# Kernel tuning notes

Measured on AMD Instinct MI355X. Metric: run time of the kernel, lower is better.

## Reference

```python
import jax, jax.numpy as jnp
import numpy as np

N_NODES, N_EDGES, F_IN = 8192, 32768, 16
N_SUB, N_GRAPH = 512, 32
EDGE_DIM, HID = 5, 128
DIMS = [(16, 32), (32, 64), (64, 64)]  # (M_in, M_out) per NNConv layer


def _segment_mean(x, seg, n):
    s = jax.ops.segment_sum(x, seg, num_segments=n)
    c = jax.ops.segment_sum(jnp.ones((x.shape[0], 1), x.dtype), seg, num_segments=n)
    return s / jnp.maximum(c, 1.0)


def _nnconv(x, src, dst, eattr, W1, b1, W2, b2, root, bias):
    # edge MLP -> per-edge weight matrix theta: [E, M_in, M_out]
    h = jax.nn.relu(eattr @ W1 + b1)
    theta = (h @ W2 + b2).reshape(-1, x.shape[1], root.shape[1])
    msg = jnp.einsum('ei,eio->eo', x[src], theta)          # gather + per-edge matvec
    agg = jax.ops.segment_sum(msg, dst, num_segments=x.shape[0])  # scatter-add (aggr='add')
    return agg + x @ root + bias


def setup_inputs() -> dict:
    key = jax.random.key(0)
    ks = jax.random.split(key, 32)
    inp = {}
    inp['x'] = jax.random.normal(ks[0], (N_NODES, F_IN), jnp.float32)
    inp['edge_index'] = jax.random.randint(ks[1], (2, N_EDGES), 0, N_NODES)
    inp['edge_attr'] = jax.random.uniform(ks[2], (N_EDGES, EDGE_DIM), jnp.float32)
    inp['node_to_subgraph'] = jnp.sort(jax.random.randint(ks[3], (N_NODES,), 0, N_SUB))
    inp['subgraph_to_graph'] = jnp.sort(jax.random.randint(ks[4], (N_SUB,), 0, N_GRAPH))
    i = 5
    for l, (ci, co) in enumerate(DIMS):
        inp[f'W1_{l}'] = jax.random.normal(ks[i], (EDGE_DIM, HID), jnp.float32) * 0.1
        inp[f'b1_{l}'] = jnp.zeros((HID,), jnp.float32)
        inp[f'W2_{l}'] = jax.random.normal(ks[i + 1], (HID, ci * co), jnp.float32) * 0.05
        inp[f'b2_{l}'] = jnp.zeros((ci * co,), jnp.float32)
        inp[f'root_{l}'] = jax.random.normal(ks[i + 2], (ci, co), jnp.float32) * 0.1
        inp[f'bias_{l}'] = jnp.zeros((co,), jnp.float32)
        i += 3
    inp['fc1_w'] = jax.random.normal(ks[i], (64, 32), jnp.float32) * 0.1
    inp['fc1_b'] = jnp.zeros((32,), jnp.float32)
    inp['fc2_w'] = jax.random.normal(ks[i + 1], (32, 16), jnp.float32) * 0.1
    inp['fc2_b'] = jnp.zeros((16,), jnp.float32)
    inp['fc3_w'] = jax.random.normal(ks[i + 2], (16, 1), jnp.float32) * 0.1
    inp['fc3_b'] = jnp.zeros((1,), jnp.float32)
    return inp


def reference(x, edge_index, edge_attr, node_to_subgraph, subgraph_to_graph,
              W1_0, b1_0, W2_0, b2_0, root_0, bias_0,
              W1_1, b1_1, W2_1, b2_1, root_1, bias_1,
              W1_2, b1_2, W2_2, b2_2, root_2, bias_2,
              fc1_w, fc1_b, fc2_w, fc2_b, fc3_w, fc3_b):
    src, dst = edge_index[0], edge_index[1]
    layers = [(W1_0, b1_0, W2_0, b2_0, root_0, bias_0),
              (W1_1, b1_1, W2_1, b2_1, root_1, bias_1),
              (W1_2, b1_2, W2_2, b2_2, root_2, bias_2)]
    h = x
    for (W1, b1, W2, b2, root, bias) in layers:
        h = jax.nn.elu(_nnconv(h, src, dst, edge_attr, W1, b1, W2, b2, root, bias))
    h = _segment_mean(h, node_to_subgraph, N_SUB)      # global_mean_pool over subgraphs
    h = _segment_mean(h, subgraph_to_graph, N_GRAPH)   # global_mean_pool over graphs
    h = jax.nn.elu(h @ fc1_w + fc1_b)
    h = jax.nn.elu(h @ fc2_w + fc2_b)
    return (h @ fc3_w + fc3_b).reshape(-1)
```

## Files before the change

kernel.cpp:

```cpp
#include <hip/hip_runtime.h>

#define E_EDGES 32768
#define NN 8192
#define HID 128

typedef _Float16 half8 __attribute__((ext_vector_type(8)));
typedef _Float16 half4 __attribute__((ext_vector_type(4)));
typedef float f32x4 __attribute__((ext_vector_type(4)));

__device__ __forceinline__ void prep_one(int idx, int l2ci, int l2co,
                                         const float* __restrict__ W2,
                                         const float* __restrict__ b2,
                                         _Float16* __restrict__ out) {
  int CI = 1 << l2ci, CO = 1 << l2co;
  int Kmain = CI << 7;
  int j = idx & 7;
  int n = (idx >> 3) & (CO - 1);
  int kg = idx >> (3 + l2co);
  int k = kg * 8 + j;
  float v = 0.f;
  if (k < Kmain) {
    int hh = k >> l2ci, i = k & (CI - 1);
    v = W2[((hh << l2ci) + i) * CO + n];
  } else if (k < Kmain + CI) {
    v = b2[(k - Kmain) * CO + n];
  }
  out[idx] = (_Float16)v;
}

#define ZTOT (8192 * 32 + 8192 * 64 + 8192 * 64 + 512 * 64)
#define PREP0 (2176 * 32)
#define PREP1 (4224 * 64)
#define PREP2 (8320 * 64)

__global__ void prep_k(float* __restrict__ zr,
                       const float* __restrict__ W2a, const float* __restrict__ b2a, _Float16* __restrict__ oa,
                       const float* __restrict__ W2b, const float* __restrict__ b2b, _Float16* __restrict__ ob,
                       const float* __restrict__ W2c, const float* __restrict__ b2c, _Float16* __restrict__ oc) {
  int idx = blockIdx.x * 256 + threadIdx.x;
  if (idx < ZTOT) { zr[idx] = 0.f; return; }
  idx -= ZTOT;
  if (idx < PREP0) prep_one(idx, 4, 5, W2a, b2a, oa);
  else if (idx < PREP0 + PREP1) prep_one(idx - PREP0, 5, 6, W2b, b2b, ob);
  else if (idx < PREP0 + PREP1 + PREP2) prep_one(idx - PREP0 - PREP1, 6, 6, W2c, b2c, oc);
}

template <int CI, int CO>
__launch_bounds__(256, 2)
__global__ void msg_mfma_k(const float* __restrict__ xcur, const int* __restrict__ src,
                           const int* __restrict__ dst, const float* __restrict__ eattr,
                           const float* __restrict__ W1, const float* __restrict__ b1,
                           const _Float16* __restrict__ Bsw, float* __restrict__ agg) {
  constexpr int ME = 256;
  constexpr int L2CI = (CI == 64) ? 6 : ((CI == 32) ? 5 : 4);
  constexpr int Kmain = 128 * CI;
  constexpr int SPLITK = 32 * CI;
  constexpr int TAILK = ((SPLITK + CI + 127) / 128) * 128;
  constexpr int XSTR = CI + 8;
  constexpr int FC = CO / 16;
  constexpr int C4 = CI / 4;
  constexpr int L2C4 = L2CI - 2;
  constexpr int NV = (CI == 64) ? 2 : 1;

  __shared__ _Float16 he_s[32 * ME];
  __shared__ _Float16 xs_s[ME * XSTR];
  __shared__ float ea_s[ME * 5];
  __shared__ float W1s[5 * 32];
  __shared__ float b1s[32];
  __shared__ int src_s[ME];
  __shared__ int dst_s[ME];

  int t = threadIdx.x;
  int e0 = blockIdx.x * ME;
  int y = blockIdx.y;
  int hbeg = y * 32;

  for (int j = t; j < ME * 5; j += 256) ea_s[j] = eattr[e0 * 5 + j];
  if (t < 5 * 32) W1s[t] = W1[(t >> 5) * HID + hbeg + (t & 31)];
  if (t < 32) b1s[t] = b1[hbeg + t];
  src_s[t] = src[e0 + t];
  dst_s[t] = dst[e0 + t];
  __syncthreads();

  for (int j = t; j < 32 * ME; j += 256) {
    int hl = j >> 8, e = j & (ME - 1);
    float v = b1s[hl];
#pragma unroll
    for (int d = 0; d < 5; ++d) v += ea_s[e * 5 + d] * W1s[d * 32 + hl];
    he_s[hl * ME + e] = (_Float16)fmaxf(v, 0.f);
  }
  for (int j = t; j < ME * C4; j += 256) {
    int e = j >> L2C4, i4 = j & (C4 - 1);
    float4 v = ((const float4*)xcur)[src_s[e] * C4 + i4];
    half4 hq = {(_Float16)v.x, (_Float16)v.y, (_Float16)v.z, (_Float16)v.w};
    *(half4*)&xs_s[e * XSTR + i4 * 4] = hq;
  }
  __syncthreads();

  int lane = t & 63;
  int w = t >> 6;
  int quad = lane >> 4, l15 = lane & 15;

  half8 xreg[4][NV];
#pragma unroll
  for (int fr = 0; fr < 4; ++fr)
#pragma unroll
    for (int v = 0; v < NV; ++v)
      xreg[fr][v] = *(const half8*)&xs_s[(w * 64 + fr * 16 + l15) * XSTR +
                                         ((quad * 8 + v * 32) & (CI - 1))];

  int cbeg = y * (SPLITK / 32);
  int cend = cbeg + ((y < 3) ? (SPLITK / 32) : (TAILK / 32));
  int nrounds = (cend - cbeg) >> 2;

  const half8* bsw8 = (const half8*)Bsw;
  int ib = quad * CO + l15;

  f32x4 acc[4][FC];
#pragma unroll
  for (int fr = 0; fr < 4; ++fr)
#pragma unroll
    for (int fc = 0; fc < FC; ++fc)
#pragma unroll
      for (int r = 0; r < 4; ++r) acc[fr][fc][r] = 0.f;

  half8 breg[4][FC];
#pragma unroll
  for (int j = 0; j < 4; ++j)
#pragma unroll
    for (int fc = 0; fc < FC; ++fc)
      breg[j][fc] = bsw8[(cbeg + j) * 4 * CO + ib + fc * 16];

  for (int r = 0; r < nrounds; ++r) {
#pragma unroll
    for (int j = 0; j < 4; ++j) {
      int c = cbeg + r * 4 + j;
      int kq = c * 32 + quad * 8;
      int hr = (kq < Kmain) ? ((kq >> L2CI) - hbeg) : 0;
      constexpr int PAR = (CI == 64) ? 1 : 0;
      int vi = PAR ? (j & 1) : 0;
      half8 a[4];
#pragma unroll
      for (int fr = 0; fr < 4; ++fr) {
        int e = w * 64 + fr * 16 + l15;
        _Float16 hv = (kq < Kmain) ? he_s[hr * ME + e] : (_Float16)1.f;
        a[fr] = xreg[fr][vi] * hv;
      }
#pragma unroll
      for (int fc = 0; fc < FC; ++fc) {
#pragma unroll
        for (int fr = 0; fr < 4; ++fr)
          acc[fr][fc] = __builtin_amdgcn_mfma_f32_16x16x32_f16(a[fr], breg[j][fc], acc[fr][fc], 0, 0, 0);
      }
      int cn = c + 4;
      if (cn >= cend) cn = cend - 1;
#pragma unroll
      for (int fc = 0; fc < FC; ++fc)
        breg[j][fc] = bsw8[cn * 4 * CO + ib + fc * 16];
    }
  }

#pragma unroll
  for (int fr = 0; fr < 4; ++fr)
#pragma unroll
    for (int r = 0; r < 4; ++r) {
      int el = w * 64 + fr * 16 + quad * 4 + r;
      int d = dst_s[el];
      float* base = agg + (size_t)d * CO + l15;
#pragma unroll
      for (int fc = 0; fc < FC; ++fc)
        atomicAdd(base + fc * 16, acc[fr][fc][r]);
    }
}

template <int CI, int CO, bool POOL>
__global__ void fin_k(const float* __restrict__ xcur, const float* __restrict__ root,
                      const float* __restrict__ bias, const float* __restrict__ agg,
                      const int* __restrict__ n2s, float* __restrict__ ssum,
                      float* __restrict__ xnext) {
  constexpr int NB = 256 / CO;
  __shared__ float xs[NB * CI];
  int t = threadIdx.x;
  int n0 = blockIdx.x * NB;
  for (int j = t; j < NB * CI; j += 256) xs[j] = xcur[n0 * CI + j];
  __syncthreads();
  int nl = t / CO, o = t & (CO - 1);
  int n = n0 + nl;
  float a = bias[o] + agg[n * CO + o];
#pragma unroll
  for (int i = 0; i < CI; ++i) a += xs[nl * CI + i] * root[i * CO + o];
  float r = a > 0.f ? a : expm1f(a);
  if (POOL) atomicAdd(&ssum[(n2s[n] << 6) + o], r);
  else xnext[n * CO + o] = r;
}

__device__ __forceinline__ int lbound(const int* __restrict__ a, int n, int v) {
  int lo = 0, hi = n;
  while (lo < hi) { int m = (lo + hi) >> 1; if (a[m] < v) lo = m + 1; else hi = m; }
  return lo;
}

__global__ void final_k(const float* __restrict__ ssum, const int* __restrict__ n2s,
                        const int* __restrict__ s2g,
                        const float* __restrict__ w1, const float* __restrict__ b1,
                        const float* __restrict__ w2, const float* __restrict__ b2,
                        const float* __restrict__ w3, const float* __restrict__ b3,
                        float* __restrict__ out) {
  __shared__ float gsum[32 * 64];
  __shared__ float cnt_s[512];
  __shared__ float gcnt[32];
  __shared__ float s1[32 * 32];
  __shared__ float s2[32 * 16];
  int t = threadIdx.x;
  for (int j = t; j < 32 * 64; j += 1024) gsum[j] = 0.f;
  if (t < 512) cnt_s[t] = (float)(lbound(n2s, NN, t + 1) - lbound(n2s, NN, t));
  if (t < 32) gcnt[t] = (float)(lbound(s2g, 512, t + 1) - lbound(s2g, 512, t));
  __syncthreads();
  for (int j = t; j < 512 * 64; j += 1024) {
    int s = j >> 6, o = j & 63;
    float v = ssum[j] / fmaxf(cnt_s[s], 1.f);
    atomicAdd(&gsum[(s2g[s] << 6) + o], v);
  }
  __syncthreads();
  for (int j = t; j < 2048; j += 1024) gsum[j] /= fmaxf(gcnt[j >> 6], 1.f);
  __syncthreads();
  {
    int g = t >> 5, jj = t & 31;
    float a = b1[jj];
    for (int i = 0; i < 64; ++i) a += gsum[(g << 6) + i] * w1[i * 32 + jj];
    s1[(g << 5) + jj] = a > 0.f ? a : expm1f(a);
  }
  __syncthreads();
  if (t < 512) {
    int g = t >> 4, jj = t & 15;
    float a = b2[jj];
    for (int i = 0; i < 32; ++i) a += s1[(g << 5) + i] * w2[i * 16 + jj];
    s2[(g << 4) + jj] = a > 0.f ? a : expm1f(a);
  }
  __syncthreads();
  if (t < 32) {
    float a = b3[0];
    for (int i = 0; i < 16; ++i) a += s2[(t << 4) + i] * w3[i];
    out[t] = a;
  }
}

extern "C" void kernel_launch(void* const* d_in, const int* in_sizes, int n_in,
                              void* d_out, int out_size, void* d_ws, size_t ws_size,
                              hipStream_t stream) {
  (void)in_sizes; (void)n_in; (void)out_size; (void)ws_size;
  const float* x0 = (const float*)d_in[0];
  const int* ei = (const int*)d_in[1];
  const float* ea = (const float*)d_in[2];
  const int* n2s = (const int*)d_in[3];
  const int* s2g = (const int*)d_in[4];
  const float* W1_[3] = {(const float*)d_in[5], (const float*)d_in[11], (const float*)d_in[17]};
  const float* b1_[3] = {(const float*)d_in[6], (const float*)d_in[12], (const float*)d_in[18]};
  const float* W2_[3] = {(const float*)d_in[7], (const float*)d_in[13], (const float*)d_in[19]};
  const float* b2_[3] = {(const float*)d_in[8], (const float*)d_in[14], (const float*)d_in[20]};
  const float* rt_[3] = {(const float*)d_in[9], (const float*)d_in[15], (const float*)d_in[21]};
  const float* bs_[3] = {(const float*)d_in[10], (const float*)d_in[16], (const float*)d_in[22]};
  const float* fc1w = (const float*)d_in[23]; const float* fc1b = (const float*)d_in[24];
  const float* fc2w = (const float*)d_in[25]; const float* fc2b = (const float*)d_in[26];
  const float* fc3w = (const float*)d_in[27]; const float* fc3b = (const float*)d_in[28];
  float* out = (float*)d_out;

  const int* srcp = ei;
  const int* dstp = ei + E_EDGES;

  char* wsb = (char*)d_ws;
  size_t off = 0;
  auto alloc = [&](size_t bytes) {
    void* p = wsb + off;
    off += (bytes + 255) & ~(size_t)255;
    return p;
  };
  _Float16* Bsw0 = (_Float16*)alloc((size_t)PREP0 * 2);
  _Float16* Bsw1 = (_Float16*)alloc((size_t)PREP1 * 2);
  _Float16* Bsw2 = (_Float16*)alloc((size_t)PREP2 * 2);
  float* agg1 = (float*)alloc((size_t)NN * 32 * 4);
  float* agg2 = (float*)alloc((size_t)NN * 64 * 4);
  float* agg3 = (float*)alloc((size_t)NN * 64 * 4);
  float* ssum = (float*)alloc((size_t)512 * 64 * 4);
  float* x1 = (float*)alloc((size_t)NN * 32 * 4);
  float* x2 = (float*)alloc((size_t)NN * 64 * 4);

  const int preptot = ZTOT + PREP0 + PREP1 + PREP2;
  prep_k<<<(preptot + 255) / 256, 256, 0, stream>>>(agg1, W2_[0], b2_[0], Bsw0,
                                                    W2_[1], b2_[1], Bsw1,
                                                    W2_[2], b2_[2], Bsw2);

  dim3 mg(E_EDGES / 256, 4);
  msg_mfma_k<16, 32><<<mg, 256, 0, stream>>>(x0, srcp, dstp, ea, W1_[0], b1_[0], Bsw0, agg1);
  fin_k<16, 32, false><<<NN / 8, 256, 0, stream>>>(x0, rt_[0], bs_[0], agg1, n2s, ssum, x1);
  msg_mfma_k<32, 64><<<mg, 256, 0, stream>>>(x1, srcp, dstp, ea, W1_[1], b1_[1], Bsw1, agg2);
  fin_k<32, 64, false><<<NN / 4, 256, 0, stream>>>(x1, rt_[1], bs_[1], agg2, n2s, ssum, x2);
  msg_mfma_k<64, 64><<<mg, 256, 0, stream>>>(x2, srcp, dstp, ea, W1_[2], b1_[2], Bsw2, agg3);
  fin_k<64, 64, true><<<NN / 4, 256, 0, stream>>>(x2, rt_[2], bs_[2], agg3, n2s, ssum, nullptr);

  final_k<<<1, 1024, 0, stream>>>(ssum, n2s, s2g, fc1w, fc1b, fc2w, fc2b, fc3w, fc3b, out);
}
```

Measured before the change: 308.0 us.

## Transpose edge-hidden buffer, hoist per-window reads, and parallelize pooling head across graphs

Stores the per-edge hidden activations edge-major so each lane loads eight hidden values with one vector read per window, instead of one scalar LDS read per K-chunk. The K loop is restructured into windows with the bias tail handled as a separate epilogue for the last split. Subgraph node counts are now accumulated atomically in the first finalize kernel. The single-block final kernel, with its binary searches and shared atomics, is replaced by a 32-block head kernel that handles one graph per block. The extra atomic per node and the fixed tail handling must exactly match the prepared weight layout.

```diff
diff --git a/kernel.cpp b/kernel.cpp
--- a/kernel.cpp
+++ b/kernel.cpp
@@ -28,7 +28,7 @@
   out[idx] = (_Float16)v;
 }
 
-#define ZTOT (8192 * 32 + 8192 * 64 + 8192 * 64 + 512 * 64)
+#define ZTOT (8192 * 32 + 8192 * 64 + 8192 * 64 + 512 * 64 + 512)
 #define PREP0 (2176 * 32)
 #define PREP1 (4224 * 64)
 #define PREP2 (8320 * 64)
@@ -53,16 +53,16 @@
                            const _Float16* __restrict__ Bsw, float* __restrict__ agg) {
   constexpr int ME = 256;
   constexpr int L2CI = (CI == 64) ? 6 : ((CI == 32) ? 5 : 4);
-  constexpr int Kmain = 128 * CI;
-  constexpr int SPLITK = 32 * CI;
-  constexpr int TAILK = ((SPLITK + CI + 127) / 128) * 128;
   constexpr int XSTR = CI + 8;
   constexpr int FC = CO / 16;
   constexpr int C4 = CI / 4;
   constexpr int L2C4 = L2CI - 2;
   constexpr int NV = (CI == 64) ? 2 : 1;
-
-  __shared__ _Float16 he_s[32 * ME];
+  constexpr int HS = 40;
+  constexpr int CW = CI / 4;
+  constexpr int RR = CW / 4;
+
+  __shared__ _Float16 he_t[ME * HS];
   __shared__ _Float16 xs_s[ME * XSTR];
   __shared__ float ea_s[ME * 5];
   __shared__ float W1s[5 * 32];
@@ -87,7 +87,7 @@
     float v = b1s[hl];
 #pragma unroll
     for (int d = 0; d < 5; ++d) v += ea_s[e * 5 + d] * W1s[d * 32 + hl];
-    he_s[hl * ME + e] = (_Float16)fmaxf(v, 0.f);
+    he_t[e * HS + hl] = (_Float16)fmaxf(v, 0.f);
   }
   for (int j = t; j < ME * C4; j += 256) {
     int e = j >> L2C4, i4 = j & (C4 - 1);
@@ -109,9 +109,8 @@
       xreg[fr][v] = *(const half8*)&xs_s[(w * 64 + fr * 16 + l15) * XSTR +
                                          ((quad * 8 + v * 32) & (CI - 1))];
 
-  int cbeg = y * (SPLITK / 32);
-  int cend = cbeg + ((y < 3) ? (SPLITK / 32) : (TAILK / 32));
-  int nrounds = (cend - cbeg) >> 2;
+  int cbeg = y * CI;
+  int ctail_end = cbeg + CI + ((y == 3) ? 4 : 0);
 
   const half8* bsw8 = (const half8*)Bsw;
   int ib = quad * CO + l15;
@@ -131,32 +130,56 @@
     for (int fc = 0; fc < FC; ++fc)
       breg[j][fc] = bsw8[(cbeg + j) * 4 * CO + ib + fc * 16];
 
-  for (int r = 0; r < nrounds; ++r) {
+  for (int win = 0; win < 4; ++win) {
+    half8 hreg[4];
+#pragma unroll
+    for (int fr = 0; fr < 4; ++fr)
+      hreg[fr] = *(const half8*)&he_t[(w * 64 + fr * 16 + l15) * HS + win * 8];
+#pragma unroll
+    for (int rr = 0; rr < RR; ++rr) {
+#pragma unroll
+      for (int j = 0; j < 4; ++j) {
+        int cl = win * CW + rr * 4 + j;
+        int c = cbeg + cl;
+        constexpr int PAR = (CI == 64) ? 1 : 0;
+        int vi = PAR ? (cl & 1) : 0;
+        half8 a[4];
+#pragma unroll
+        for (int fr = 0; fr < 4; ++fr) {
+          _Float16 hv;
+          if (CI == 16)      hv = (quad & 2) ? hreg[fr][2 * j + 1] : hreg[fr][2 * j];
+          else if (CI == 32) hv = hreg[fr][rr * 4 + j];
+          else               hv = hreg[fr][(rr * 4 + j) >> 1];
+          half8 hb = {hv, hv, hv, hv, hv, hv, hv, hv};
+          a[fr] = xreg[fr][vi] * hb;
+        }
+#pragma unroll
+        for (int fc = 0; fc < FC; ++fc) {
+#pragma unroll
+          for (int fr = 0; fr < 4; ++fr)
+            acc[fr][fc] = __builtin_amdgcn_mfma_f32_16x16x32_f16(a[fr], breg[cl & 3][fc], acc[fr][fc], 0, 0, 0);
+        }
+        int cn = c + 4;
+        if (cn >= ctail_end) cn = ctail_end - 1;
+#pragma unroll
+        for (int fc = 0; fc < FC; ++fc)
+          breg[cl & 3][fc] = bsw8[cn * 4 * CO + ib + fc * 16];
+      }
+    }
+  }
+
+  if (y == 3) {
 #pragma unroll
     for (int j = 0; j < 4; ++j) {
-      int c = cbeg + r * 4 + j;
-      int kq = c * 32 + quad * 8;
-      int hr = (kq < Kmain) ? ((kq >> L2CI) - hbeg) : 0;
+      int cl = CI + j;
       constexpr int PAR = (CI == 64) ? 1 : 0;
-      int vi = PAR ? (j & 1) : 0;
-      half8 a[4];
-#pragma unroll
-      for (int fr = 0; fr < 4; ++fr) {
-        int e = w * 64 + fr * 16 + l15;
-        _Float16 hv = (kq < Kmain) ? he_s[hr * ME + e] : (_Float16)1.f;
-        a[fr] = xreg[fr][vi] * hv;
+      int vi = PAR ? (cl & 1) : 0;
+#pragma unroll
+      for (int fc = 0; fc < FC; ++fc) {
+#pragma unroll
+        for (int fr = 0; fr < 4; ++fr)
+          acc[fr][fc] = __builtin_amdgcn_mfma_f32_16x16x32_f16(xreg[fr][vi], breg[cl & 3][fc], acc[fr][fc], 0, 0, 0);
       }
-#pragma unroll
-      for (int fc = 0; fc < FC; ++fc) {
-#pragma unroll
-        for (int fr = 0; fr < 4; ++fr)
-          acc[fr][fc] = __builtin_amdgcn_mfma_f32_16x16x32_f16(a[fr], breg[j][fc], acc[fr][fc], 0, 0, 0);
-      }
-      int cn = c + 4;
-      if (cn >= cend) cn = cend - 1;
-#pragma unroll
-      for (int fc = 0; fc < FC; ++fc)
-        breg[j][fc] = bsw8[cn * 4 * CO + ib + fc * 16];
     }
   }
 
@@ -173,11 +196,11 @@
     }
 }
 
-template <int CI, int CO, bool POOL>
+template <int CI, int CO, bool POOL, bool CNT>
 __global__ void fin_k(const float* __restrict__ xcur, const float* __restrict__ root,
                       const float* __restrict__ bias, const float* __restrict__ agg,
-                      const int* __restrict__ n2s, float* __restrict__ ssum,
-                      float* __restrict__ xnext) {
+                      const int* __restrict__ n2s, int* __restrict__ cnt_sub,
+                      float* __restrict__ ssum, float* __restrict__ xnext) {
   constexpr int NB = 256 / CO;
   __shared__ float xs[NB * CI];
   int t = threadIdx.x;
@@ -190,6 +213,7 @@
 #pragma unroll
   for (int i = 0; i < CI; ++i) a += xs[nl * CI + i] * root[i * CO + o];
   float r = a > 0.f ? a : expm1f(a);
+  if (CNT && o == 0) atomicAdd(&cnt_sub[n2s[n]], 1);
   if (POOL) atomicAdd(&ssum[(n2s[n] << 6) + o], r);
   else xnext[n * CO + o] = r;
 }
@@ -200,48 +224,38 @@
   return lo;
 }
 
-__global__ void final_k(const float* __restrict__ ssum, const int* __restrict__ n2s,
-                        const int* __restrict__ s2g,
-                        const float* __restrict__ w1, const float* __restrict__ b1,
-                        const float* __restrict__ w2, const float* __restrict__ b2,
-                        const float* __restrict__ w3, const float* __restrict__ b3,
-                        float* __restrict__ out) {
-  __shared__ float gsum[32 * 64];
-  __shared__ float cnt_s[512];
-  __shared__ float gcnt[32];
-  __shared__ float s1[32 * 32];
-  __shared__ float s2[32 * 16];
+__global__ void head_k(const float* __restrict__ ssum, const int* __restrict__ cnt_sub,
+                       const int* __restrict__ s2g,
+                       const float* __restrict__ w1, const float* __restrict__ b1,
+                       const float* __restrict__ w2, const float* __restrict__ b2,
+                       const float* __restrict__ w3, const float* __restrict__ b3,
+                       float* __restrict__ out) {
+  int g = blockIdx.x;
   int t = threadIdx.x;
-  for (int j = t; j < 32 * 64; j += 1024) gsum[j] = 0.f;
-  if (t < 512) cnt_s[t] = (float)(lbound(n2s, NN, t + 1) - lbound(n2s, NN, t));
-  if (t < 32) gcnt[t] = (float)(lbound(s2g, 512, t + 1) - lbound(s2g, 512, t));
-  __syncthreads();
-  for (int j = t; j < 512 * 64; j += 1024) {
-    int s = j >> 6, o = j & 63;
-    float v = ssum[j] / fmaxf(cnt_s[s], 1.f);
-    atomicAdd(&gsum[(s2g[s] << 6) + o], v);
-  }
-  __syncthreads();
-  for (int j = t; j < 2048; j += 1024) gsum[j] /= fmaxf(gcnt[j >> 6], 1.f);
-  __syncthreads();
-  {
-    int g = t >> 5, jj = t & 31;
-    float a = b1[jj];
-    for (int i = 0; i < 64; ++i) a += gsum[(g << 6) + i] * w1[i * 32 + jj];
-    s1[(g << 5) + jj] = a > 0.f ? a : expm1f(a);
-  }
-  __syncthreads();
-  if (t < 512) {
-    int g = t >> 4, jj = t & 15;
-    float a = b2[jj];
-    for (int i = 0; i < 32; ++i) a += s1[(g << 5) + i] * w2[i * 16 + jj];
-    s2[(g << 4) + jj] = a > 0.f ? a : expm1f(a);
-  }
+  __shared__ float m[64], s1[32], s2[16];
+  int slo = lbound(s2g, 512, g);
+  int shi = lbound(s2g, 512, g + 1);
+  float acc = 0.f;
+  for (int s = slo; s < shi; ++s)
+    acc += ssum[(s << 6) + t] / fmaxf((float)cnt_sub[s], 1.f);
+  m[t] = acc / fmaxf((float)(shi - slo), 1.f);
   __syncthreads();
   if (t < 32) {
+    float a = b1[t];
+    for (int i = 0; i < 64; ++i) a += m[i] * w1[i * 32 + t];
+    s1[t] = a > 0.f ? a : expm1f(a);
+  }
+  __syncthreads();
+  if (t < 16) {
+    float a = b2[t];
+    for (int i = 0; i < 32; ++i) a += s1[i] * w2[i * 16 + t];
+    s2[t] = a > 0.f ? a : expm1f(a);
+  }
+  __syncthreads();
+  if (t == 0) {
     float a = b3[0];
-    for (int i = 0; i < 16; ++i) a += s2[(t << 4) + i] * w3[i];
-    out[t] = a;
+    for (int i = 0; i < 16; ++i) a += s2[i] * w3[i];
+    out[g] = a;
   }
 }
 
@@ -282,6 +296,7 @@
   float* agg2 = (float*)alloc((size_t)NN * 64 * 4);
   float* agg3 = (float*)alloc((size_t)NN * 64 * 4);
   float* ssum = (float*)alloc((size_t)512 * 64 * 4);
+  int* cnt_sub = (int*)alloc((size_t)512 * 4);
   float* x1 = (float*)alloc((size_t)NN * 32 * 4);
   float* x2 = (float*)alloc((size_t)NN * 64 * 4);
 
@@ -292,11 +307,11 @@
 
   dim3 mg(E_EDGES / 256, 4);
   msg_mfma_k<16, 32><<<mg, 256, 0, stream>>>(x0, srcp, dstp, ea, W1_[0], b1_[0], Bsw0, agg1);
-  fin_k<16, 32, false><<<NN / 8, 256, 0, stream>>>(x0, rt_[0], bs_[0], agg1, n2s, ssum, x1);
+  fin_k<16, 32, false, true><<<NN / 8, 256, 0, stream>>>(x0, rt_[0], bs_[0], agg1, n2s, cnt_sub, ssum, x1);
   msg_mfma_k<32, 64><<<mg, 256, 0, stream>>>(x1, srcp, dstp, ea, W1_[1], b1_[1], Bsw1, agg2);
-  fin_k<32, 64, false><<<NN / 4, 256, 0, stream>>>(x1, rt_[1], bs_[1], agg2, n2s, ssum, x2);
+  fin_k<32, 64, false, false><<<NN / 4, 256, 0, stream>>>(x1, rt_[1], bs_[1], agg2, n2s, cnt_sub, ssum, x2);
   msg_mfma_k<64, 64><<<mg, 256, 0, stream>>>(x2, srcp, dstp, ea, W1_[2], b1_[2], Bsw2, agg3);
-  fin_k<64, 64, true><<<NN / 4, 256, 0, stream>>>(x2, rt_[2], bs_[2], agg3, n2s, ssum, nullptr);
-
-  final_k<<<1, 1024, 0, stream>>>(ssum, n2s, s2g, fc1w, fc1b, fc2w, fc2b, fc3w, fc3b, out);
-}
+  fin_k<64, 64, true, false><<<NN / 4, 256, 0, stream>>>(x2, rt_[2], bs_[2], agg3, n2s, cnt_sub, ssum, nullptr);
+
+  head_k<<<32, 64, 0, stream>>>(ssum, cnt_sub, s2g, fc1w, fc1b, fc2w, fc2b, fc3w, fc3b, out);
+}
```

New measurement: 282.6 us. -8.3%, faster.
